# Kernel tuning notes

Measured on AMD Instinct MI355X. Metric: run time of the kernel, lower is better.

The kernel has to match this reference:

```python
import jax, jax.numpy as jnp
import numpy as np

JOINT_NUM = 25   # len(smpl_x.pos_joint_part['body'])
HM_D, HM_H, HM_W = 8, 8, 8
FEAT_DIM = 768


def setup_inputs() -> dict:
    key = jax.random.key(0)
    k1, k2, k3 = jax.random.split(key, 3)
    B = 512
    img_feat = jax.random.normal(k1, (B, FEAT_DIM, HM_H, HM_W), dtype=jnp.float32)
    out_ch = JOINT_NUM * HM_D  # 200
    # Conv2d 1x1 weight [out_ch, in_ch] and bias [out_ch]
    scale = 1.0 / np.sqrt(FEAT_DIM)
    conv_w = jax.random.uniform(k2, (out_ch, FEAT_DIM), jnp.float32, -scale, scale)
    conv_b = jax.random.uniform(k3, (out_ch,), jnp.float32, -scale, scale)
    return {"img_feat": img_feat, "conv_w": conv_w, "conv_b": conv_b}


def reference(img_feat, conv_w, conv_b):
    B = img_feat.shape[0]
    # 1x1 conv == per-pixel matmul over channels: bchw,oc -> bohw
    hm = jnp.einsum('bchw,oc->bohw', img_feat, conv_w) + conv_b[None, :, None, None]
    joint_hm_logits = hm.reshape(B, JOINT_NUM, HM_D, HM_H, HM_W)
    # softmax over flattened D*H*W
    flat = joint_hm_logits.reshape(B, JOINT_NUM, HM_D * HM_H * HM_W)
    p = jax.nn.softmax(flat, axis=2).reshape(B, JOINT_NUM, HM_D, HM_H, HM_W)
    # soft-argmax: marginal expectations along each axis
    accu_x = p.sum(axis=(2, 3))  # [B, J, W]
    accu_y = p.sum(axis=(2, 4))  # [B, J, H]
    accu_z = p.sum(axis=(3, 4))  # [B, J, D]
    x = (accu_x * jnp.arange(HM_W, dtype=jnp.float32)).sum(axis=2, keepdims=True)
    y = (accu_y * jnp.arange(HM_H, dtype=jnp.float32)).sum(axis=2, keepdims=True)
    z = (accu_z * jnp.arange(HM_D, dtype=jnp.float32)).sum(axis=2, keepdims=True)
    joint_coord = jnp.concatenate((x, y, z), axis=2)  # [B, J, 3]
    # original recomputes the same softmax for the returned heatmap
    joint_hm = p
    return (joint_hm, joint_coord)
```

## Files before the change

kernel.cpp:

```cpp
#include <hip/hip_runtime.h>


typedef __attribute__((ext_vector_type(4))) float f32x4;
typedef __attribute__((ext_vector_type(8))) short bf16x8;
typedef __attribute__((ext_vector_type(4))) unsigned short us4;
typedef __attribute__((ext_vector_type(4))) unsigned int u32x4;

namespace {
constexpr int kB = 512, kC = 768, kP = 64, kO = 200, kJ = 25;
constexpr int kKT = 64, kSteps = 12;
constexpr int kNT = 13, kNTP = 14;
constexpr int kWsHalf = 12 * 2 * 14 * 512;
constexpr size_t kHmOut = (size_t)kB * kJ * 512;
}

__device__ inline unsigned short f2bf(float x) {
  union { float f; unsigned u; } c; c.f = x;
  unsigned r = c.u + 0x7FFFu + ((c.u >> 16) & 1u);
  return (unsigned short)(r >> 16);
}
__device__ inline float bf2f(unsigned short h) {
  union { unsigned u; float f; } c; c.u = ((unsigned)h) << 16;
  return c.f;
}

__global__ __launch_bounds__(256) void weight_split_kernel(
    const float* __restrict__ w, unsigned short* __restrict__ ws) {
  const int id = blockIdx.x * 256 + threadIdx.x;
  if (id >= 43008) return;
  const int ml = id & 15, g = (id >> 4) & 3;
  const int id2 = id >> 6;
  const int nt = id2 % 14;
  const int q = id2 / 14;
  const int kc = q & 1;
  const int q2 = q >> 1;
  const int t = q2 % 12;
  const int half = q2 / 12;
  const int n = nt * 16 + ml;
  const int kb = t * 64 + kc * 32 + g * 8;
  float v[8];
#pragma unroll
  for (int i = 0; i < 8; ++i)
    v[i] = (n < kO) ? w[(size_t)n * kC + kb + i] : 0.f;
  unsigned short o8[8];
#pragma unroll
  for (int i = 0; i < 8; ++i) {
    const unsigned short hi = f2bf(v[i]);
    o8[i] = half ? f2bf(v[i] - bf2f(hi)) : hi;
  }
  unsigned short* dst =
      ws + (size_t)half * kWsHalf +
      ((((size_t)(t * 2 + kc) * 14 + nt) * 4 + g) * 16 + ml) * 8;
  *(us4*)dst = us4{o8[0], o8[1], o8[2], o8[3]};
  *(us4*)(dst + 4) = us4{o8[4], o8[5], o8[6], o8[7]};
}

__device__ inline int afrag(int buf, int half, int kc, int g, int px) {
  return ((((buf * 2 + half) * 2 + kc) * 4 + g) * 64 + px) * 16;
}

__global__ __launch_bounds__(256, 3) void gemm_kernel(
    const float* __restrict__ img, const unsigned short* __restrict__ wsb,
    const float* __restrict__ bias, float* __restrict__ out) {
  __shared__ __align__(16) char smem[32768];

  const int b = blockIdx.x;
  const int tid = threadIdx.x;
  const int lane = tid & 63;
  const int wid = tid >> 6;
  const int m_l = lane & 15;
  const int g = lane >> 4;
  const float* __restrict__ imgb = img + (size_t)b * kC * kP;

  const int px = lane;
  const int c0 = wid * 16;
  const int skc = c0 >> 5;
  const int sg0 = (c0 & 31) >> 3;

  f32x4 acc[4][4];
#pragma unroll
  for (int i = 0; i < 4; ++i)
#pragma unroll
    for (int j = 0; j < 4; ++j) acc[i][j] = f32x4{0.f, 0.f, 0.f, 0.f};

  float pf[16];

  auto load_pf = [&](int t) {
#pragma unroll
    for (int i = 0; i < 16; ++i)
      pf[i] = imgb[(size_t)(t * kKT + c0 + i) * kP + px];
  };
  auto split_write = [&](int buf) {
    unsigned ph[8], pl[8];
#pragma unroll
    for (int i = 0; i < 8; ++i) {
      const unsigned a = __float_as_uint(pf[2 * i]);
      const unsigned c = __float_as_uint(pf[2 * i + 1]);
      const unsigned am = a & 0xFFFF0000u, cm = c & 0xFFFF0000u;
      ph[i] = (a >> 16) | cm;
      const float la = __uint_as_float(a) - __uint_as_float(am);
      const float lc = __uint_as_float(c) - __uint_as_float(cm);
      pl[i] = (__float_as_uint(la) >> 16) | (__float_as_uint(lc) & 0xFFFF0000u);
    }
    *(u32x4*)(smem + afrag(buf, 0, skc, sg0, px)) = u32x4{ph[0], ph[1], ph[2], ph[3]};
    *(u32x4*)(smem + afrag(buf, 0, skc, sg0 + 1, px)) = u32x4{ph[4], ph[5], ph[6], ph[7]};
    *(u32x4*)(smem + afrag(buf, 1, skc, sg0, px)) = u32x4{pl[0], pl[1], pl[2], pl[3]};
    *(u32x4*)(smem + afrag(buf, 1, skc, sg0 + 1, px)) = u32x4{pl[4], pl[5], pl[6], pl[7]};
  };

  load_pf(0);
  split_write(0);
  __syncthreads();

  for (int t = 0; t < kSteps; ++t) {
    const int buf = t & 1;
    if (t + 1 < kSteps) load_pf(t + 1);

#pragma unroll
    for (int kc = 0; kc < 2; ++kc) {
      bf16x8 ah[4], al[4];
#pragma unroll
      for (int mt = 0; mt < 4; ++mt) {
        ah[mt] = *(const bf16x8*)(smem + afrag(buf, 0, kc, g, mt * 16 + m_l));
        al[mt] = *(const bf16x8*)(smem + afrag(buf, 1, kc, g, mt * 16 + m_l));
      }
#pragma unroll
      for (int ni = 0; ni < 4; ++ni) {
        const int nt = ni * 4 + wid;
        if (nt < kNT) {
          const unsigned short* bp =
              wsb + ((size_t)(t * 2 + kc) * 14 + nt) * 512 + lane * 8;
          const bf16x8 bh = *(const bf16x8*)bp;
          const bf16x8 bl = *(const bf16x8*)(bp + kWsHalf);
#pragma unroll
          for (int mt = 0; mt < 4; ++mt) {
            acc[ni][mt] = __builtin_amdgcn_mfma_f32_16x16x32_bf16(
                ah[mt], bh, acc[ni][mt], 0, 0, 0);
            acc[ni][mt] = __builtin_amdgcn_mfma_f32_16x16x32_bf16(
                ah[mt], bl, acc[ni][mt], 0, 0, 0);
            acc[ni][mt] = __builtin_amdgcn_mfma_f32_16x16x32_bf16(
                al[mt], bh, acc[ni][mt], 0, 0, 0);
          }
        }
      }
    }
    __syncthreads();
    if (t + 1 < kSteps) split_write(buf ^ 1);
    __syncthreads();
  }

#pragma unroll
  for (int ni = 0; ni < 4; ++ni) {
    const int nt = ni * 4 + wid;
    if (nt < kNT) {
      const int o = nt * 16 + m_l;
      if (o < kO) {
        const float bo = bias[o];
#pragma unroll
        for (int mt = 0; mt < 4; ++mt) {
          f32x4 v;
#pragma unroll
          for (int r = 0; r < 4; ++r) v[r] = acc[ni][mt][r] + bo;
          *(f32x4*)(out + ((size_t)b * kO + o) * 64 + mt * 16 + g * 4) = v;
        }
      }
    }
  }
}

__global__ __launch_bounds__(256) void softmax_kernel(float* __restrict__ out) {
  const int b = blockIdx.x;
  const int j = blockIdx.y * 4 + (threadIdx.x >> 6);
  const int lane = threadIdx.x & 63;
  if (j >= kJ) return;

  float* base = out + ((size_t)b * kJ + j) * 512;
  float v[8];
#pragma unroll
  for (int k = 0; k < 8; ++k) v[k] = base[k * 64 + lane];

  float m = v[0];
#pragma unroll
  for (int k = 1; k < 8; ++k) m = fmaxf(m, v[k]);
#pragma unroll
  for (int off = 32; off > 0; off >>= 1) m = fmaxf(m, __shfl_xor(m, off));

  float e[8];
  float s = 0.f;
#pragma unroll
  for (int k = 0; k < 8; ++k) {
    e[k] = __expf(v[k] - m);
    s += e[k];
  }
#pragma unroll
  for (int off = 32; off > 0; off >>= 1) s += __shfl_xor(s, off);
  const float inv = 1.0f / s;

  float psum = 0.f, zsum = 0.f;
#pragma unroll
  for (int k = 0; k < 8; ++k) {
    const float pv = e[k] * inv;
    base[k * 64 + lane] = pv;
    psum += pv;
    zsum += (float)k * pv;
  }
  float xs = (float)(lane & 7) * psum;
  float ys = (float)(lane >> 3) * psum;
#pragma unroll
  for (int off = 32; off > 0; off >>= 1) {
    xs += __shfl_xor(xs, off);
    ys += __shfl_xor(ys, off);
    zsum += __shfl_xor(zsum, off);
  }
  if (lane == 0) {
    float* cd = out + kHmOut + ((size_t)b * kJ + j) * 3;
    cd[0] = xs;
    cd[1] = ys;
    cd[2] = zsum;
  }
}

extern "C" void kernel_launch(void* const* d_in, const int* in_sizes, int n_in,
                              void* d_out, int out_size, void* d_ws,
                              size_t ws_size, hipStream_t stream) {
  const float* img = (const float*)d_in[0];
  const float* w = (const float*)d_in[1];
  const float* bias = (const float*)d_in[2];
  unsigned short* wsb = (unsigned short*)d_ws;
  float* out = (float*)d_out;

  weight_split_kernel<<<dim3(168), dim3(256), 0, stream>>>(w, wsb);
  gemm_kernel<<<dim3(kB), dim3(256), 0, stream>>>(img, wsb, bias, out);
  softmax_kernel<<<dim3(kB, 7), dim3(256), 0, stream>>>(out);
}
```

Baseline: 199.4 us.

## Fuse GEMM with softmax via LDS staging and switch to single-pass fp16 MFMA

Drops the three-pass bf16 hi/lo split emulation of fp32 and uses a single fp16 MFMA pass, with inputs and weights converted to half. The GEMM and softmax/soft-argmax kernels are merged: logits are staged in LDS with padded rows and the softmax runs from LDS. This removes the global round trip of the logits and one launch. Blocks grow to 512 threads, and one barrier per K step is removed by writing into the alternate buffer. fp16 has less exponent range and less accuracy than the split scheme, which risks tolerance failures.

```diff
diff --git a/kernel.cpp b/kernel.cpp
--- a/kernel.cpp
+++ b/kernel.cpp
@@ -2,221 +2,174 @@
 
 
 typedef __attribute__((ext_vector_type(4))) float f32x4;
-typedef __attribute__((ext_vector_type(8))) short bf16x8;
-typedef __attribute__((ext_vector_type(4))) unsigned short us4;
-typedef __attribute__((ext_vector_type(4))) unsigned int u32x4;
+typedef _Float16 f16x8 __attribute__((ext_vector_type(8)));
+typedef unsigned short us8 __attribute__((ext_vector_type(8)));
 
 namespace {
 constexpr int kB = 512, kC = 768, kP = 64, kO = 200, kJ = 25;
-constexpr int kKT = 64, kSteps = 12;
-constexpr int kNT = 13, kNTP = 14;
-constexpr int kWsHalf = 12 * 2 * 14 * 512;
+constexpr int kSteps = 12;
+constexpr int kNT = 13;
+constexpr int kHR = 65;
+constexpr int kWsFrag8 = 12 * 2 * 14 * 64;
 constexpr size_t kHmOut = (size_t)kB * kJ * 512;
+constexpr int kSmemBytes = kO * kHR * 4;
 }
 
-__device__ inline unsigned short f2bf(float x) {
-  union { float f; unsigned u; } c; c.f = x;
-  unsigned r = c.u + 0x7FFFu + ((c.u >> 16) & 1u);
-  return (unsigned short)(r >> 16);
-}
-__device__ inline float bf2f(unsigned short h) {
-  union { unsigned u; float f; } c; c.u = ((unsigned)h) << 16;
-  return c.f;
-}
-
-__global__ __launch_bounds__(256) void weight_split_kernel(
+__global__ __launch_bounds__(256) void weight_half_kernel(
     const float* __restrict__ w, unsigned short* __restrict__ ws) {
   const int id = blockIdx.x * 256 + threadIdx.x;
-  if (id >= 43008) return;
+  if (id >= kWsFrag8) return;
   const int ml = id & 15, g = (id >> 4) & 3;
   const int id2 = id >> 6;
   const int nt = id2 % 14;
   const int q = id2 / 14;
-  const int kc = q & 1;
-  const int q2 = q >> 1;
-  const int t = q2 % 12;
-  const int half = q2 / 12;
   const int n = nt * 16 + ml;
-  const int kb = t * 64 + kc * 32 + g * 8;
-  float v[8];
-#pragma unroll
-  for (int i = 0; i < 8; ++i)
-    v[i] = (n < kO) ? w[(size_t)n * kC + kb + i] : 0.f;
-  unsigned short o8[8];
+  const int kb = q * 32 + g * 8;
+  union { _Float16 h[8]; us8 u; } pk;
 #pragma unroll
   for (int i = 0; i < 8; ++i) {
-    const unsigned short hi = f2bf(v[i]);
-    o8[i] = half ? f2bf(v[i] - bf2f(hi)) : hi;
+    const float v = (n < kO) ? w[(size_t)n * kC + kb + i] : 0.f;
+    pk.h[i] = (_Float16)v;
   }
-  unsigned short* dst =
-      ws + (size_t)half * kWsHalf +
-      ((((size_t)(t * 2 + kc) * 14 + nt) * 4 + g) * 16 + ml) * 8;
-  *(us4*)dst = us4{o8[0], o8[1], o8[2], o8[3]};
-  *(us4*)(dst + 4) = us4{o8[4], o8[5], o8[6], o8[7]};
+  *(us8*)(ws + (size_t)id * 8) = pk.u;
 }
 
-__device__ inline int afrag(int buf, int half, int kc, int g, int px) {
-  return ((((buf * 2 + half) * 2 + kc) * 4 + g) * 64 + px) * 16;
+__device__ inline int acell(int buf, int kc, int g, int px) {
+  return (((buf * 2 + kc) * 4 + g) * 64 + px) * 8;
 }
 
-__global__ __launch_bounds__(256, 3) void gemm_kernel(
+__global__ __launch_bounds__(512, 4) void posnet_fused_kernel(
     const float* __restrict__ img, const unsigned short* __restrict__ wsb,
     const float* __restrict__ bias, float* __restrict__ out) {
-  __shared__ __align__(16) char smem[32768];
+  __shared__ __align__(16) char smem[kSmemBytes];
+  unsigned short* aLds = (unsigned short*)smem;
+  float* hm = (float*)smem;
 
   const int b = blockIdx.x;
   const int tid = threadIdx.x;
   const int lane = tid & 63;
   const int wid = tid >> 6;
+  const int ng = __builtin_amdgcn_readfirstlane(wid & 3);
+  const int mh = __builtin_amdgcn_readfirstlane(wid >> 2);
   const int m_l = lane & 15;
   const int g = lane >> 4;
   const float* __restrict__ imgb = img + (size_t)b * kC * kP;
 
-  const int px = lane;
-  const int c0 = wid * 16;
-  const int skc = c0 >> 5;
-  const int sg0 = (c0 & 31) >> 3;
+  const int sc0 = wid * 8;
+  const int skc = sc0 >> 5;
+  const int sg = (sc0 & 31) >> 3;
 
-  f32x4 acc[4][4];
+  f32x4 acc[4][2];
 #pragma unroll
   for (int i = 0; i < 4; ++i)
 #pragma unroll
-    for (int j = 0; j < 4; ++j) acc[i][j] = f32x4{0.f, 0.f, 0.f, 0.f};
+    for (int j = 0; j < 2; ++j) acc[i][j] = f32x4{0.f, 0.f, 0.f, 0.f};
 
-  float pf[16];
-
+  float pf[8];
   auto load_pf = [&](int t) {
 #pragma unroll
-    for (int i = 0; i < 16; ++i)
-      pf[i] = imgb[(size_t)(t * kKT + c0 + i) * kP + px];
+    for (int i = 0; i < 8; ++i)
+      pf[i] = imgb[(size_t)(t * 64 + sc0 + i) * kP + lane];
   };
-  auto split_write = [&](int buf) {
-    unsigned ph[8], pl[8];
+  auto cvt_write = [&](int buf) {
+    union { _Float16 h[8]; us8 u; } pk;
 #pragma unroll
-    for (int i = 0; i < 8; ++i) {
-      const unsigned a = __float_as_uint(pf[2 * i]);
-      const unsigned c = __float_as_uint(pf[2 * i + 1]);
-      const unsigned am = a & 0xFFFF0000u, cm = c & 0xFFFF0000u;
-      ph[i] = (a >> 16) | cm;
-      const float la = __uint_as_float(a) - __uint_as_float(am);
-      const float lc = __uint_as_float(c) - __uint_as_float(cm);
-      pl[i] = (__float_as_uint(la) >> 16) | (__float_as_uint(lc) & 0xFFFF0000u);
-    }
-    *(u32x4*)(smem + afrag(buf, 0, skc, sg0, px)) = u32x4{ph[0], ph[1], ph[2], ph[3]};
-    *(u32x4*)(smem + afrag(buf, 0, skc, sg0 + 1, px)) = u32x4{ph[4], ph[5], ph[6], ph[7]};
-    *(u32x4*)(smem + afrag(buf, 1, skc, sg0, px)) = u32x4{pl[0], pl[1], pl[2], pl[3]};
-    *(u32x4*)(smem + afrag(buf, 1, skc, sg0 + 1, px)) = u32x4{pl[4], pl[5], pl[6], pl[7]};
+    for (int i = 0; i < 8; ++i) pk.h[i] = (_Float16)pf[i];
+    *(us8*)(aLds + acell(buf, skc, sg, lane)) = pk.u;
   };
 
   load_pf(0);
-  split_write(0);
+  cvt_write(0);
   __syncthreads();
 
   for (int t = 0; t < kSteps; ++t) {
     const int buf = t & 1;
     if (t + 1 < kSteps) load_pf(t + 1);
-
 #pragma unroll
     for (int kc = 0; kc < 2; ++kc) {
-      bf16x8 ah[4], al[4];
+      const f16x8 a0 = *(const f16x8*)(aLds + acell(buf, kc, g, mh * 32 + m_l));
+      const f16x8 a1 =
+          *(const f16x8*)(aLds + acell(buf, kc, g, mh * 32 + 16 + m_l));
 #pragma unroll
-      for (int mt = 0; mt < 4; ++mt) {
-        ah[mt] = *(const bf16x8*)(smem + afrag(buf, 0, kc, g, mt * 16 + m_l));
-        al[mt] = *(const bf16x8*)(smem + afrag(buf, 1, kc, g, mt * 16 + m_l));
-      }
-#pragma unroll
-      for (int ni = 0; ni < 4; ++ni) {
-        const int nt = ni * 4 + wid;
+      for (int ii = 0; ii < 4; ++ii) {
+        const int nt = ii * 4 + ng;
         if (nt < kNT) {
-          const unsigned short* bp =
-              wsb + ((size_t)(t * 2 + kc) * 14 + nt) * 512 + lane * 8;
-          const bf16x8 bh = *(const bf16x8*)bp;
-          const bf16x8 bl = *(const bf16x8*)(bp + kWsHalf);
-#pragma unroll
-          for (int mt = 0; mt < 4; ++mt) {
-            acc[ni][mt] = __builtin_amdgcn_mfma_f32_16x16x32_bf16(
-                ah[mt], bh, acc[ni][mt], 0, 0, 0);
-            acc[ni][mt] = __builtin_amdgcn_mfma_f32_16x16x32_bf16(
-                ah[mt], bl, acc[ni][mt], 0, 0, 0);
-            acc[ni][mt] = __builtin_amdgcn_mfma_f32_16x16x32_bf16(
-                al[mt], bh, acc[ni][mt], 0, 0, 0);
-          }
+          const f16x8 bb = *(const f16x8*)(
+              wsb + ((size_t)(t * 2 + kc) * 14 + nt) * 512 + lane * 8);
+          acc[ii][0] =
+              __builtin_amdgcn_mfma_f32_16x16x32_f16(a0, bb, acc[ii][0], 0, 0, 0);
+          acc[ii][1] =
+              __builtin_amdgcn_mfma_f32_16x16x32_f16(a1, bb, acc[ii][1], 0, 0, 0);
         }
       }
     }
-    __syncthreads();
-    if (t + 1 < kSteps) split_write(buf ^ 1);
+    if (t + 1 < kSteps) cvt_write((t + 1) & 1);
     __syncthreads();
   }
 
 #pragma unroll
-  for (int ni = 0; ni < 4; ++ni) {
-    const int nt = ni * 4 + wid;
+  for (int ii = 0; ii < 4; ++ii) {
+    const int nt = ii * 4 + ng;
     if (nt < kNT) {
       const int o = nt * 16 + m_l;
       if (o < kO) {
         const float bo = bias[o];
 #pragma unroll
-        for (int mt = 0; mt < 4; ++mt) {
-          f32x4 v;
+        for (int mt = 0; mt < 2; ++mt) {
+          const int m = (mh * 2 + mt) * 16 + g * 4;
 #pragma unroll
-          for (int r = 0; r < 4; ++r) v[r] = acc[ni][mt][r] + bo;
-          *(f32x4*)(out + ((size_t)b * kO + o) * 64 + mt * 16 + g * 4) = v;
+          for (int r = 0; r < 4; ++r) hm[o * kHR + m + r] = acc[ii][mt][r] + bo;
         }
       }
     }
   }
-}
+  __syncthreads();
 
-__global__ __launch_bounds__(256) void softmax_kernel(float* __restrict__ out) {
-  const int b = blockIdx.x;
-  const int j = blockIdx.y * 4 + (threadIdx.x >> 6);
-  const int lane = threadIdx.x & 63;
-  if (j >= kJ) return;
+  for (int j = wid; j < kJ; j += 8) {
+    float v[8];
+#pragma unroll
+    for (int k = 0; k < 8; ++k) v[k] = hm[(j * 8 + k) * kHR + lane];
 
-  float* base = out + ((size_t)b * kJ + j) * 512;
-  float v[8];
+    float m = v[0];
 #pragma unroll
-  for (int k = 0; k < 8; ++k) v[k] = base[k * 64 + lane];
+    for (int k = 1; k < 8; ++k) m = fmaxf(m, v[k]);
+#pragma unroll
+    for (int off = 32; off > 0; off >>= 1) m = fmaxf(m, __shfl_xor(m, off));
 
-  float m = v[0];
+    float e[8];
+    float s = 0.f;
 #pragma unroll
-  for (int k = 1; k < 8; ++k) m = fmaxf(m, v[k]);
+    for (int k = 0; k < 8; ++k) {
+      e[k] = __expf(v[k] - m);
+      s += e[k];
+    }
 #pragma unroll
-  for (int off = 32; off > 0; off >>= 1) m = fmaxf(m, __shfl_xor(m, off));
+    for (int off = 32; off > 0; off >>= 1) s += __shfl_xor(s, off);
+    const float inv = 1.0f / s;
 
-  float e[8];
-  float s = 0.f;
+    float psum = 0.f, zsum = 0.f;
+    float* dst = out + ((size_t)b * kJ + j) * 512;
 #pragma unroll
-  for (int k = 0; k < 8; ++k) {
-    e[k] = __expf(v[k] - m);
-    s += e[k];
-  }
+    for (int k = 0; k < 8; ++k) {
+      const float pv = e[k] * inv;
+      dst[k * 64 + lane] = pv;
+      psum += pv;
+      zsum += (float)k * pv;
+    }
+    float xs = (float)(lane & 7) * psum;
+    float ys = (float)(lane >> 3) * psum;
 #pragma unroll
-  for (int off = 32; off > 0; off >>= 1) s += __shfl_xor(s, off);
-  const float inv = 1.0f / s;
-
-  float psum = 0.f, zsum = 0.f;
-#pragma unroll
-  for (int k = 0; k < 8; ++k) {
-    const float pv = e[k] * inv;
-    base[k * 64 + lane] = pv;
-    psum += pv;
-    zsum += (float)k * pv;
-  }
-  float xs = (float)(lane & 7) * psum;
-  float ys = (float)(lane >> 3) * psum;
-#pragma unroll
-  for (int off = 32; off > 0; off >>= 1) {
-    xs += __shfl_xor(xs, off);
-    ys += __shfl_xor(ys, off);
-    zsum += __shfl_xor(zsum, off);
-  }
-  if (lane == 0) {
-    float* cd = out + kHmOut + ((size_t)b * kJ + j) * 3;
-    cd[0] = xs;
-    cd[1] = ys;
-    cd[2] = zsum;
+    for (int off = 32; off > 0; off >>= 1) {
+      xs += __shfl_xor(xs, off);
+      ys += __shfl_xor(ys, off);
+      zsum += __shfl_xor(zsum, off);
+    }
+    if (lane == 0) {
+      float* cd = out + kHmOut + ((size_t)b * kJ + j) * 3;
+      cd[0] = xs;
+      cd[1] = ys;
+      cd[2] = zsum;
+    }
   }
 }
 
@@ -229,7 +182,6 @@
   unsigned short* wsb = (unsigned short*)d_ws;
   float* out = (float*)d_out;
 
-  weight_split_kernel<<<dim3(168), dim3(256), 0, stream>>>(w, wsb);
-  gemm_kernel<<<dim3(kB), dim3(256), 0, stream>>>(img, wsb, bias, out);
-  softmax_kernel<<<dim3(kB, 7), dim3(256), 0, stream>>>(out);
+  weight_half_kernel<<<dim3((kWsFrag8 + 255) / 256), dim3(256), 0, stream>>>(w, wsb);
+  posnet_fused_kernel<<<dim3(kB), dim3(512), 0, stream>>>(img, wsb, bias, out);
 }
```

New measurement: 170.7 us. -14.4%, faster.
